# Performance work log

Hardware: AMD Instinct MI355X
Metric: run time of the kernel (lower is better)

The kernel has to match this reference:

```python
import jax, jax.numpy as jnp
import numpy as np

D_MODEL = 512
NHEAD = 8
DK = D_MODEL // NHEAD
DIM_FF = 2048
LN_EPS = 1e-5


def setup_inputs() -> dict:
    key = jax.random.key(0)
    ks = jax.random.split(key, 12)
    B, L = 8, 1024
    s = 1.0 / np.sqrt(D_MODEL)
    sf = 1.0 / np.sqrt(DIM_FF)
    return {
        "x": jax.random.normal(ks[0], (B, L, D_MODEL), jnp.float32),
        "key_padding_mask": jnp.zeros((B, L), dtype=bool),
        "bias": jax.random.normal(ks[1], (B, L, L), jnp.float32),
        # projection weights stored [in, out] so y = x @ W + b (matches torch Linear math)
        "Wq": jax.random.normal(ks[2], (D_MODEL, D_MODEL), jnp.float32) * s,
        "bq": jnp.zeros((D_MODEL,), jnp.float32),
        "Wk": jax.random.normal(ks[3], (D_MODEL, D_MODEL), jnp.float32) * s,
        "bk": jnp.zeros((D_MODEL,), jnp.float32),
        "Wv": jax.random.normal(ks[4], (D_MODEL, D_MODEL), jnp.float32) * s,
        "bv": jnp.zeros((D_MODEL,), jnp.float32),
        "Wo": jax.random.normal(ks[5], (D_MODEL, D_MODEL), jnp.float32) * s,
        "bo": jnp.zeros((D_MODEL,), jnp.float32),
        "ln1_g": jnp.ones((D_MODEL,), jnp.float32),
        "ln1_b": jnp.zeros((D_MODEL,), jnp.float32),
        "W1": jax.random.normal(ks[6], (D_MODEL, DIM_FF), jnp.float32) * s,
        "b1": jnp.zeros((DIM_FF,), jnp.float32),
        "W2": jax.random.normal(ks[7], (DIM_FF, D_MODEL), jnp.float32) * sf,
        "b2": jnp.zeros((D_MODEL,), jnp.float32),
        "ln2_g": jnp.ones((D_MODEL,), jnp.float32),
        "ln2_b": jnp.zeros((D_MODEL,), jnp.float32),
    }


def _layernorm(x, g, b):
    mu = jnp.mean(x, axis=-1, keepdims=True)
    var = jnp.mean(jnp.square(x - mu), axis=-1, keepdims=True)
    return (x - mu) * jax.lax.rsqrt(var + LN_EPS) * g + b


def reference(x, key_padding_mask, bias, Wq, bq, Wk, bk, Wv, bv, Wo, bo,
              ln1_g, ln1_b, W1, b1, W2, b2, ln2_g, ln2_b):
    B, L, H = x.shape
    residual = x
    # [B, L, D] -> [B, nhead, L, dk]
    q = (x @ Wq + bq).reshape(B, L, NHEAD, DK).transpose(0, 2, 1, 3)
    k = (x @ Wk + bk).reshape(B, L, NHEAD, DK).transpose(0, 2, 1, 3)
    v = (x @ Wv + bv).reshape(B, L, NHEAD, DK).transpose(0, 2, 1, 3)
    scores = jnp.einsum("bhqd,bhkd->bhqk", q, k) / np.sqrt(DK)
    scores = scores + bias[:, None, :, :]
    scores = jnp.where(key_padding_mask[:, None, None, :], -jnp.inf, scores)
    attn = jax.nn.softmax(scores, axis=-1)  # dropout p=0 (eval)
    out = jnp.einsum("bhqk,bhkd->bhqd", attn, v)
    out = out.transpose(0, 2, 1, 3).reshape(B, L, H)
    out = out @ Wo + bo
    x = _layernorm(residual + out, ln1_g, ln1_b)
    residual = x
    h = jax.nn.relu(x @ W1 + b1)
    x = h @ W2 + b2
    return _layernorm(residual + x, ln2_g, ln2_b)
```

## Files before the change

kernel.cpp:

```cpp
#include <hip/hip_runtime.h>
#include <math.h>

#define NHEAD 8
#define DKD 64
#define DMODEL 512
#define LSEQ 1024
#define NBL 8192

typedef __attribute__((ext_vector_type(8))) short bf8;
typedef __attribute__((ext_vector_type(4))) float f4;

__device__ inline unsigned short f2bf(float f) {
    union { float f; unsigned u; } v; v.f = f;
    unsigned r = v.u + 0x7FFFu + ((v.u >> 16) & 1u);
    return (unsigned short)(r >> 16);
}

__device__ __forceinline__ unsigned cvtpk(float lo, float hi) {
    unsigned r;
    asm("v_cvt_pk_bf16_f32 %0, %1, %2" : "=v"(r) : "v"(lo), "v"(hi));
    return r;
}

__device__ __forceinline__ void gload16(const void* g, void* l) {
    __builtin_amdgcn_global_load_lds(
        (const __attribute__((address_space(1))) unsigned int*)g,
        (__attribute__((address_space(3))) unsigned int*)l, 16, 0, 0);
}

__global__ __launch_bounds__(256) void conv_bf16(
    const float* __restrict__ in, unsigned short* __restrict__ out, int n)
{
    int i = (blockIdx.x * 256 + threadIdx.x) * 4;
    if (i >= n) return;
    float4 v = *(const float4*)(in + i);
    ushort4 o;
    o.x = f2bf(v.x); o.y = f2bf(v.y); o.z = f2bf(v.z); o.w = f2bf(v.w);
    *(ushort4*)(out + i) = o;
}

__global__ __launch_bounds__(256) void biasmb_kernel(
    const float* __restrict__ bias, const unsigned char* __restrict__ mask,
    unsigned short* __restrict__ o)
{
    size_t flat = ((size_t)blockIdx.x * 256 + threadIdx.x) * 8;
    int b = (int)(flat >> 20);
    int k = (int)(flat & 1023);
    float4 v0 = *(const float4*)(bias + flat);
    float4 v1 = *(const float4*)(bias + flat + 4);
    uint2 mk = *(const uint2*)(mask + b * 1024 + k);
    float vs[8] = {v0.x, v0.y, v0.z, v0.w, v1.x, v1.y, v1.z, v1.w};
    unsigned mw[2] = {mk.x, mk.y};
    unsigned short os[8];
    #pragma unroll
    for (int j = 0; j < 8; ++j) {
        unsigned mb = (mw[j >> 2] >> ((j & 3) * 8)) & 0xffu;
        os[j] = f2bf(mb ? -1e30f : vs[j]);
    }
    uint4 pk;
    pk.x = (unsigned)os[0] | ((unsigned)os[1] << 16);
    pk.y = (unsigned)os[2] | ((unsigned)os[3] << 16);
    pk.z = (unsigned)os[4] | ((unsigned)os[5] << 16);
    pk.w = (unsigned)os[6] | ((unsigned)os[7] << 16);
    *(uint4*)(o + flat) = pk;
}

__device__ __forceinline__ void do_transpose(
    const float* __restrict__ W, unsigned short* __restrict__ Wt,
    int K, int N, int bx, int by)
{
    __shared__ float tile[64][65];
    const int k0 = by * 64, n0 = bx * 64;
    const int c = threadIdx.x & 63, r0 = (threadIdx.x >> 6) * 16;
    #pragma unroll
    for (int i = 0; i < 16; ++i)
        tile[r0 + i][c] = W[(size_t)(k0 + r0 + i) * N + n0 + c];
    __syncthreads();
    #pragma unroll
    for (int i = 0; i < 16; ++i)
        Wt[(size_t)(n0 + r0 + i) * K + k0 + c] = f2bf(tile[c][r0 + i]);
}

__global__ __launch_bounds__(256) void prep_weights(
    const float* __restrict__ Wq, const float* __restrict__ Wk,
    const float* __restrict__ Wv, const float* __restrict__ Wo,
    const float* __restrict__ W1, const float* __restrict__ W2,
    const float* __restrict__ bq, const float* __restrict__ bk,
    const float* __restrict__ bv,
    unsigned short* __restrict__ Wqkv, unsigned short* __restrict__ Wot,
    unsigned short* __restrict__ W1t, unsigned short* __restrict__ W2t,
    float* __restrict__ bqkv)
{
    int j = blockIdx.x;
    if (j < 256) {
        int which = j >> 6, tt = j & 63;
        const float* src = which == 0 ? Wq : which == 1 ? Wk : which == 2 ? Wv : Wo;
        unsigned short* dst = which == 0 ? Wqkv : which == 1 ? (Wqkv + 262144)
                            : which == 2 ? (Wqkv + 524288) : Wot;
        do_transpose(src, dst, 512, 512, tt & 7, tt >> 3);
    } else if (j < 512) {
        int tt = j - 256;
        do_transpose(W1, W1t, 512, 2048, tt & 31, tt >> 5);
    } else if (j < 768) {
        int tt = j - 512;
        do_transpose(W2, W2t, 2048, 512, tt & 7, tt >> 3);
    } else {
        for (int c = threadIdx.x; c < 1536; c += 256)
            bqkv[c] = c < 512 ? bq[c] : c < 1024 ? bk[c - 512] : bv[c - 1024];
    }
}

template<int BN>
__global__ __launch_bounds__(256) void mfma_gemm(
    const unsigned short* __restrict__ A, const unsigned short* __restrict__ Bt,
    const float* __restrict__ bias, const float* __restrict__ resid,
    void* __restrict__ outp, int M, int N, int K, int relu, int outmode,
    unsigned short* __restrict__ qs, unsigned short* __restrict__ ks,
    unsigned short* __restrict__ vts)
{
    __shared__ uint4 As[2][1024];
    __shared__ uint4 Bs[2][BN * 8];
    constexpr int NB = BN / 32;

    const int t = threadIdx.x;
    const int lane = t & 63, w = t >> 6;
    const int g = lane >> 4, r15 = lane & 15;
    const int wr = w >> 1, wc = w & 1;

    const int nwg  = gridDim.x * gridDim.y;
    const int flat = blockIdx.y * gridDim.x + blockIdx.x;
    const int swz  = (flat & 7) * (nwg >> 3) + (flat >> 3);
    const int bx   = swz % gridDim.x, by = swz / gridDim.x;
    const int rowBase = by * 128, colBase = bx * BN;

    f4 acc[4][NB] = {};

    const int r   = t >> 3;
    const int chs = (t & 7) ^ (r & 7);
    const unsigned short* Ag0 = A  + (size_t)(rowBase + r) * K + chs * 8;
    const unsigned short* Bg0 = Bt + (size_t)(colBase + r) * K + chs * 8;

    auto stage = [&](int buf, int k0) {
        unsigned short* Al = (unsigned short*)As[buf] + (w * 8) * 64;
        unsigned short* Bl = (unsigned short*)Bs[buf] + (w * 8) * 64;
        const unsigned short* Ag = Ag0 + k0;
        const unsigned short* Bg = Bg0 + k0;
        #pragma unroll
        for (int p = 0; p < 4; ++p)
            gload16(Ag + (size_t)(p * 32) * K, Al + p * 32 * 64);
        #pragma unroll
        for (int p = 0; p < NB; ++p)
            gload16(Bg + (size_t)(p * 32) * K, Bl + p * 32 * 64);
    };

    const int nst = K >> 6;
    stage(0, 0);
    __syncthreads();

    for (int it = 0; it < nst; ++it) {
        const int cur = it & 1;
        if (it + 1 < nst) stage(cur ^ 1, (it + 1) << 6);
        #pragma unroll
        for (int kk = 0; kk < 2; ++kk) {
            bf8 af[4], bfr[NB];
            #pragma unroll
            for (int m = 0; m < 4; ++m) {
                int ra = wr * 64 + m * 16 + r15;
                af[m] = *(const bf8*)&As[cur][ra * 8 + ((kk * 4 + g) ^ (ra & 7))];
            }
            #pragma unroll
            for (int n = 0; n < NB; ++n) {
                int rb = wc * (BN / 2) + n * 16 + r15;
                bfr[n] = *(const bf8*)&Bs[cur][rb * 8 + ((kk * 4 + g) ^ (rb & 7))];
            }
            #pragma unroll
            for (int m = 0; m < 4; ++m)
                #pragma unroll
                for (int n = 0; n < NB; ++n)
                    acc[m][n] = __builtin_amdgcn_mfma_f32_16x16x32_bf16(
                        af[m], bfr[n], acc[m][n], 0, 0, 0);
        }
        __syncthreads();
    }

    #pragma unroll
    for (int m = 0; m < 4; ++m) {
        #pragma unroll
        for (int n = 0; n < NB; ++n) {
            int col = colBase + wc * (BN / 2) + n * 16 + r15;
            float bv = bias[col];
            #pragma unroll
            for (int rr = 0; rr < 4; ++rr) {
                int row = rowBase + wr * 64 + m * 16 + g * 4 + rr;
                float v = acc[m][n][rr] + bv;
                if (relu) v = fmaxf(v, 0.f);
                if (outmode == 0) {
                    size_t idx = (size_t)row * N + col;
                    if (resid) v += resid[idx];
                    ((float*)outp)[idx] = v;
                } else if (outmode == 1) {
                    ((unsigned short*)outp)[(size_t)row * N + col] = f2bf(v);
                } else {
                    int sel = col >> 9, hd = col & 511;
                    int h = hd >> 6, dk = hd & 63;
                    int b = row >> 10, l = row & 1023;
                    unsigned short bw = f2bf(v);
                    size_t bh = (size_t)(b * NHEAD + h);
                    if (sel == 0)      qs[(bh * LSEQ + l) * DKD + dk] = bw;
                    else if (sel == 1) ks[(bh * LSEQ + l) * DKD + dk] = bw;
                    else               vts[(bh * DKD + dk) * LSEQ + l] = bw;
                }
            }
        }
    }
}

__global__ __launch_bounds__(256) void attn_mfma(
    const unsigned short* __restrict__ Qg, const unsigned short* __restrict__ Kg,
    const unsigned short* __restrict__ Vtg, const unsigned short* __restrict__ biasMb,
    unsigned short* __restrict__ Ob)
{
    __shared__ uint4 Ks[2][512];
    __shared__ uint4 Vs[2][512];
    __shared__ uint4 Bls[2][1024];
    __shared__ unsigned int Pb[4096];

    const int t = threadIdx.x;
    const int lane = t & 63, w = t >> 6;
    const int g = lane >> 4, r15 = lane & 15;

    const int p = blockIdx.x;
    const int logical = (p & 7) * 64 + (p >> 3);
    const int bh = logical >> 3, qt = logical & 7;
    const int b = bh >> 3, h = bh & 7;
    const int qbase = qt * 128 + w * 32;

    bf8 qf[2][2];
    #pragma unroll
    for (int u = 0; u < 2; ++u) {
        const unsigned short* qp = Qg + ((size_t)bh * LSEQ + qbase + u * 16 + r15) * DKD + g * 8;
        qf[u][0] = *(const bf8*)qp;
        qf[u][1] = *(const bf8*)(qp + 32);
    }

    float mrun[2] = {-1e30f, -1e30f}, lsum[2] = {0.f, 0.f};
    f4 oacc[2][4] = {};

    const int sr   = t >> 3;
    const int chs  = (t & 7) ^ (sr & 7);
    const int brow = lane >> 3;
    const int bch  = (lane & 7) ^ brow;
    unsigned short* Pw = (unsigned short*)(Pb + w * 1024);

    const size_t kBase = (size_t)bh * LSEQ * DKD;
    const size_t vBase = (size_t)bh * DKD * LSEQ;
    const unsigned short* bB = biasMb + ((size_t)b << 20);

    auto stage = [&](int buf, int key0) {
        const unsigned short* Kgp = Kg  + kBase + (size_t)(key0 + sr) * DKD + chs * 8;
        const unsigned short* Vgp = Vtg + vBase + (size_t)sr * LSEQ + key0 + chs * 8;
        unsigned short* Kl = (unsigned short*)Ks[buf] + (w * 8) * 64;
        unsigned short* Vl = (unsigned short*)Vs[buf] + (w * 8) * 64;
        gload16(Kgp, Kl);
        gload16(Kgp + (size_t)32 * DKD, Kl + 32 * 64);
        gload16(Vgp, Vl);
        gload16(Vgp + (size_t)32 * LSEQ, Vl + 32 * 64);
        unsigned short* Bl = (unsigned short*)Bls[buf] + w * 2048;
        #pragma unroll
        for (int pp = 0; pp < 4; ++pp) {
            const unsigned short* Bgp = bB + (size_t)(qbase + pp * 8 + brow) * 1024
                                      + key0 + bch * 8;
            gload16(Bgp, Bl + pp * 512);
        }
    };

    stage(0, 0);
    __syncthreads();

    for (int kt = 0; kt < 16; ++kt) {
        const int cur = kt & 1;
        if (kt < 15) stage(cur ^ 1, (kt + 1) * 64);

        const char* Bw = (const char*)Bls[cur] + w * 4096;

        f4 sacc[2][4] = {};
        __builtin_amdgcn_s_setprio(1);
        #pragma unroll
        for (int kk = 0; kk < 2; ++kk)
            #pragma unroll
            for (int m = 0; m < 4; ++m) {
                int row = m * 16 + r15;
                bf8 kf = *(const bf8*)&Ks[cur][row * 8 + ((kk * 4 + g) ^ (row & 7))];
                sacc[0][m] = __builtin_amdgcn_mfma_f32_16x16x32_bf16(kf, qf[0][kk], sacc[0][m], 0, 0, 0);
                sacc[1][m] = __builtin_amdgcn_mfma_f32_16x16x32_bf16(kf, qf[1][kk], sacc[1][m], 0, 0, 0);
            }
        __builtin_amdgcn_s_setprio(0);

        #pragma unroll
        for (int u = 0; u < 2; ++u) {
            float s[16];
            float pmax = -1e30f;
            #pragma unroll
            for (int m = 0; m < 4; ++m) {
                int off = (u * 16 + r15) * 128 + ((m * 32 + g * 8) ^ ((r15 & 7) << 4));
                uint2 bv = *(const uint2*)(Bw + off);
                float b0 = __uint_as_float(bv.x << 16);
                float b1 = __uint_as_float(bv.x & 0xffff0000u);
                float b2 = __uint_as_float(bv.y << 16);
                float b3 = __uint_as_float(bv.y & 0xffff0000u);
                s[m * 4 + 0] = fmaf(sacc[u][m][0], 0.125f, b0);
                s[m * 4 + 1] = fmaf(sacc[u][m][1], 0.125f, b1);
                s[m * 4 + 2] = fmaf(sacc[u][m][2], 0.125f, b2);
                s[m * 4 + 3] = fmaf(sacc[u][m][3], 0.125f, b3);
                #pragma unroll
                for (int j = 0; j < 4; ++j) pmax = fmaxf(pmax, s[m * 4 + j]);
            }
            pmax = fmaxf(pmax, __shfl_xor(pmax, 16));
            pmax = fmaxf(pmax, __shfl_xor(pmax, 32));

            if (!__all(pmax <= mrun[u] + 8.f)) {
                float mnew = fmaxf(mrun[u], pmax);
                float scale = __expf(mrun[u] - mnew);
                lsum[u] *= scale;
                #pragma unroll
                for (int m = 0; m < 4; ++m)
                    #pragma unroll
                    for (int j = 0; j < 4; ++j) oacc[u][m][j] *= scale;
                mrun[u] = mnew;
            }

            float psum = 0.f;
            #pragma unroll
            for (int i = 0; i < 16; ++i) { s[i] = __expf(s[i] - mrun[u]); psum += s[i]; }
            psum += __shfl_xor(psum, 16);
            psum += __shfl_xor(psum, 32);
            lsum[u] += psum;

            #pragma unroll
            for (int m = 0; m < 4; ++m) {
                uint2 pk;
                pk.x = cvtpk(s[m * 4 + 0], s[m * 4 + 1]);
                pk.y = cvtpk(s[m * 4 + 2], s[m * 4 + 3]);
                int off = ((u * 16 + r15) * 128 + m * 32 + g * 8) ^ ((r15 & 7) << 4);
                *(uint2*)((char*)Pw + off) = pk;
            }
        }

        #pragma unroll
        for (int kk = 0; kk < 2; ++kk) {
            bf8 pf[2];
            #pragma unroll
            for (int u = 0; u < 2; ++u) {
                int off = ((u * 16 + r15) * 128 + kk * 64 + g * 16) ^ ((r15 & 7) << 4);
                pf[u] = *(const bf8*)((char*)Pw + off);
            }
            __builtin_amdgcn_s_setprio(1);
            #pragma unroll
            for (int m = 0; m < 4; ++m) {
                int row = m * 16 + r15;
                bf8 vf = *(const bf8*)&Vs[cur][row * 8 + ((kk * 4 + g) ^ (row & 7))];
                oacc[0][m] = __builtin_amdgcn_mfma_f32_16x16x32_bf16(vf, pf[0], oacc[0][m], 0, 0, 0);
                oacc[1][m] = __builtin_amdgcn_mfma_f32_16x16x32_bf16(vf, pf[1], oacc[1][m], 0, 0, 0);
            }
            __builtin_amdgcn_s_setprio(0);
        }
        __syncthreads();
    }

    #pragma unroll
    for (int u = 0; u < 2; ++u) {
        float inv = 1.f / lsum[u];
        unsigned short* op = Ob + ((size_t)b * LSEQ + qbase + u * 16 + r15) * DMODEL + h * DKD;
        #pragma unroll
        for (int m = 0; m < 4; ++m) {
            ushort4 o4;
            o4.x = f2bf(oacc[u][m][0] * inv);
            o4.y = f2bf(oacc[u][m][1] * inv);
            o4.z = f2bf(oacc[u][m][2] * inv);
            o4.w = f2bf(oacc[u][m][3] * inv);
            *(ushort4*)(op + m * 16 + g * 4) = o4;
        }
    }
}

__global__ __launch_bounds__(256) void ln_kernel(
    const float* __restrict__ in, const float* __restrict__ g,
    const float* __restrict__ bt, float* __restrict__ out,
    unsigned short* __restrict__ outb)
{
    const int row  = blockIdx.x * 4 + (threadIdx.x >> 6);
    const int lane = threadIdx.x & 63;
    const float* rp = in + (size_t)row * DMODEL + lane * 8;
    float4 x0 = *(const float4*)rp;
    float4 x1 = *(const float4*)(rp + 4);
    float xs[8] = {x0.x, x0.y, x0.z, x0.w, x1.x, x1.y, x1.z, x1.w};

    float sum = 0.f;
    #pragma unroll
    for (int i = 0; i < 8; ++i) sum += xs[i];
    #pragma unroll
    for (int off = 32; off; off >>= 1) sum += __shfl_xor(sum, off);
    float mu = sum * (1.f / 512.f);

    float vs = 0.f;
    #pragma unroll
    for (int i = 0; i < 8; ++i) { float d = xs[i] - mu; vs += d * d; }
    #pragma unroll
    for (int off = 32; off; off >>= 1) vs += __shfl_xor(vs, off);
    float rs = rsqrtf(vs * (1.f / 512.f) + 1e-5f);

    const float* gp = g  + lane * 8;
    const float* bp = bt + lane * 8;
    float4 g0 = *(const float4*)gp, g1 = *(const float4*)(gp + 4);
    float4 b0 = *(const float4*)bp, b1 = *(const float4*)(bp + 4);
    float gs[8] = {g0.x, g0.y, g0.z, g0.w, g1.x, g1.y, g1.z, g1.w};
    float bs[8] = {b0.x, b0.y, b0.z, b0.w, b1.x, b1.y, b1.z, b1.w};

    float res[8];
    #pragma unroll
    for (int i = 0; i < 8; ++i) res[i] = (xs[i] - mu) * rs * gs[i] + bs[i];

    float* op = out + (size_t)row * DMODEL + lane * 8;
    float4 r0 = {res[0], res[1], res[2], res[3]};
    float4 r1 = {res[4], res[5], res[6], res[7]};
    *(float4*)op       = r0;
    *(float4*)(op + 4) = r1;

    if (outb) {
        unsigned short* ob = outb + (size_t)row * DMODEL + lane * 8;
        ushort4 u0, u1;
        u0.x = f2bf(res[0]); u0.y = f2bf(res[1]); u0.z = f2bf(res[2]); u0.w = f2bf(res[3]);
        u1.x = f2bf(res[4]); u1.y = f2bf(res[5]); u1.z = f2bf(res[6]); u1.w = f2bf(res[7]);
        *(ushort4*)ob       = u0;
        *(ushort4*)(ob + 4) = u1;
    }
}

extern "C" void kernel_launch(void* const* d_in, const int* in_sizes, int n_in,
                              void* d_out, int out_size, void* d_ws, size_t ws_size,
                              hipStream_t stream)
{
    const float*         x    = (const float*)d_in[0];
    const unsigned char* mask = (const unsigned char*)d_in[1];
    const float*         bias = (const float*)d_in[2];
    const float* Wq = (const float*)d_in[3];
    const float* bq = (const float*)d_in[4];
    const float* Wk = (const float*)d_in[5];
    const float* bk = (const float*)d_in[6];
    const float* Wv = (const float*)d_in[7];
    const float* bv = (const float*)d_in[8];
    const float* Wo = (const float*)d_in[9];
    const float* bo = (const float*)d_in[10];
    const float* ln1g = (const float*)d_in[11];
    const float* ln1b = (const float*)d_in[12];
    const float* W1 = (const float*)d_in[13];
    const float* b1 = (const float*)d_in[14];
    const float* W2 = (const float*)d_in[15];
    const float* b2 = (const float*)d_in[16];
    const float* ln2g = (const float*)d_in[17];
    const float* ln2b = (const float*)d_in[18];

    char* W = (char*)d_ws;
    unsigned short* Qb   = (unsigned short*)(W);
    unsigned short* Kb   = (unsigned short*)(W + (8u << 20));
    unsigned short* Vtb  = (unsigned short*)(W + (16u << 20));
    unsigned short* Oball= (unsigned short*)(W + (24u << 20));
    unsigned short* hb   = (unsigned short*)(W);
    unsigned short* biasMb=(unsigned short*)(W + (32u << 20));
    float*          y12  = (float*)(W + (32u << 20));
    float*          x1   = (float*)(W + (49u << 20));
    unsigned short* xb   = (unsigned short*)(W + (66u << 20));
    unsigned short* x1b  = xb;
    unsigned short* Wqkv = (unsigned short*)(W + (74u << 20));
    unsigned short* Wot  = (unsigned short*)(W + (76u << 20));
    unsigned short* W1t  = (unsigned short*)(W + (77u << 20));
    unsigned short* W2t  = (unsigned short*)(W + (79u << 20));
    float*          bqkv = (float*)(W + (81u << 20));
    float*          outp = (float*)d_out;

    conv_bf16<<<dim3(4096), dim3(256), 0, stream>>>(x, xb, NBL * DMODEL);
    prep_weights<<<dim3(769), dim3(256), 0, stream>>>(
        Wq, Wk, Wv, Wo, W1, W2, bq, bk, bv, Wqkv, Wot, W1t, W2t, bqkv);
    biasmb_kernel<<<dim3(4096), dim3(256), 0, stream>>>(bias, mask, biasMb);

    mfma_gemm<128><<<dim3(12, 64), dim3(256), 0, stream>>>(
        xb, Wqkv, bqkv, nullptr, nullptr, NBL, 1536, 512, 0, 2, Qb, Kb, Vtb);

    attn_mfma<<<dim3(512), dim3(256), 0, stream>>>(Qb, Kb, Vtb, biasMb, Oball);

    mfma_gemm<64><<<dim3(8, 64), dim3(256), 0, stream>>>(
        Oball, Wot, bo, x, y12, NBL, 512, 512, 0, 0, nullptr, nullptr, nullptr);

    ln_kernel<<<dim3(NBL / 4), dim3(256), 0, stream>>>(y12, ln1g, ln1b, x1, x1b);

    mfma_gemm<128><<<dim3(16, 64), dim3(256), 0, stream>>>(
        x1b, W1t, b1, nullptr, hb, NBL, 2048, 512, 1, 1, nullptr, nullptr, nullptr);

    mfma_gemm<64><<<dim3(8, 64), dim3(256), 0, stream>>>(
        hb, W2t, b2, x1, y12, NBL, 512, 2048, 0, 0, nullptr, nullptr, nullptr);

    ln_kernel<<<dim3(NBL / 4), dim3(256), 0, stream>>>(y12, ln2g, ln2b, outp, nullptr);
}
```

Before: 327.9 us.

## Merge prep kernels, triple-buffer GEMM loads, and narrow GEMM tiles to BN=64

Folds the x conversion, bias/mask conversion and weight transposes into one launch, removing two kernel launches. The GEMM moves from double to triple buffering, using explicit vmcnt waits with raw s_barrier and raising wave priority around the MFMA block so loads stay further ahead of compute. The QKV and FFN1 GEMMs switch from 128-wide to 64-wide column tiles with twice as many blocks. Risks include more LDS per block, which may cut occupancy, and less reuse per narrower tile.

```diff
diff --git a/kernel.cpp b/kernel.cpp
--- a/kernel.cpp
+++ b/kernel.cpp
@@ -26,43 +26,6 @@
     __builtin_amdgcn_global_load_lds(
         (const __attribute__((address_space(1))) unsigned int*)g,
         (__attribute__((address_space(3))) unsigned int*)l, 16, 0, 0);
-}
-
-__global__ __launch_bounds__(256) void conv_bf16(
-    const float* __restrict__ in, unsigned short* __restrict__ out, int n)
-{
-    int i = (blockIdx.x * 256 + threadIdx.x) * 4;
-    if (i >= n) return;
-    float4 v = *(const float4*)(in + i);
-    ushort4 o;
-    o.x = f2bf(v.x); o.y = f2bf(v.y); o.z = f2bf(v.z); o.w = f2bf(v.w);
-    *(ushort4*)(out + i) = o;
-}
-
-__global__ __launch_bounds__(256) void biasmb_kernel(
-    const float* __restrict__ bias, const unsigned char* __restrict__ mask,
-    unsigned short* __restrict__ o)
-{
-    size_t flat = ((size_t)blockIdx.x * 256 + threadIdx.x) * 8;
-    int b = (int)(flat >> 20);
-    int k = (int)(flat & 1023);
-    float4 v0 = *(const float4*)(bias + flat);
-    float4 v1 = *(const float4*)(bias + flat + 4);
-    uint2 mk = *(const uint2*)(mask + b * 1024 + k);
-    float vs[8] = {v0.x, v0.y, v0.z, v0.w, v1.x, v1.y, v1.z, v1.w};
-    unsigned mw[2] = {mk.x, mk.y};
-    unsigned short os[8];
-    #pragma unroll
-    for (int j = 0; j < 8; ++j) {
-        unsigned mb = (mw[j >> 2] >> ((j & 3) * 8)) & 0xffu;
-        os[j] = f2bf(mb ? -1e30f : vs[j]);
-    }
-    uint4 pk;
-    pk.x = (unsigned)os[0] | ((unsigned)os[1] << 16);
-    pk.y = (unsigned)os[2] | ((unsigned)os[3] << 16);
-    pk.z = (unsigned)os[4] | ((unsigned)os[5] << 16);
-    pk.w = (unsigned)os[6] | ((unsigned)os[7] << 16);
-    *(uint4*)(o + flat) = pk;
 }
 
 __device__ __forceinline__ void do_transpose(
@@ -81,7 +44,10 @@
         Wt[(size_t)(n0 + r0 + i) * K + k0 + c] = f2bf(tile[c][r0 + i]);
 }
 
-__global__ __launch_bounds__(256) void prep_weights(
+__global__ __launch_bounds__(256) void prep_all(
+    const float* __restrict__ x, unsigned short* __restrict__ xb,
+    const float* __restrict__ bias, const unsigned char* __restrict__ mask,
+    unsigned short* __restrict__ biasMb,
     const float* __restrict__ Wq, const float* __restrict__ Wk,
     const float* __restrict__ Wv, const float* __restrict__ Wo,
     const float* __restrict__ W1, const float* __restrict__ W2,
@@ -91,22 +57,52 @@
     unsigned short* __restrict__ W1t, unsigned short* __restrict__ W2t,
     float* __restrict__ bqkv)
 {
-    int j = blockIdx.x;
-    if (j < 256) {
-        int which = j >> 6, tt = j & 63;
-        const float* src = which == 0 ? Wq : which == 1 ? Wk : which == 2 ? Wv : Wo;
-        unsigned short* dst = which == 0 ? Wqkv : which == 1 ? (Wqkv + 262144)
-                            : which == 2 ? (Wqkv + 524288) : Wot;
-        do_transpose(src, dst, 512, 512, tt & 7, tt >> 3);
-    } else if (j < 512) {
-        int tt = j - 256;
-        do_transpose(W1, W1t, 512, 2048, tt & 31, tt >> 5);
-    } else if (j < 768) {
-        int tt = j - 512;
-        do_transpose(W2, W2t, 2048, 512, tt & 7, tt >> 3);
+    const int j = blockIdx.x;
+    if (j < 4096) {
+        int i = (j * 256 + threadIdx.x) * 4;
+        float4 v = *(const float4*)(x + i);
+        ushort4 o;
+        o.x = f2bf(v.x); o.y = f2bf(v.y); o.z = f2bf(v.z); o.w = f2bf(v.w);
+        *(ushort4*)(xb + i) = o;
+    } else if (j < 8192) {
+        size_t flat = ((size_t)(j - 4096) * 256 + threadIdx.x) * 8;
+        int b = (int)(flat >> 20);
+        int k = (int)(flat & 1023);
+        float4 v0 = *(const float4*)(bias + flat);
+        float4 v1 = *(const float4*)(bias + flat + 4);
+        uint2 mk = *(const uint2*)(mask + b * 1024 + k);
+        float vs[8] = {v0.x, v0.y, v0.z, v0.w, v1.x, v1.y, v1.z, v1.w};
+        unsigned mw[2] = {mk.x, mk.y};
+        unsigned short os[8];
+        #pragma unroll
+        for (int q = 0; q < 8; ++q) {
+            unsigned mb = (mw[q >> 2] >> ((q & 3) * 8)) & 0xffu;
+            os[q] = f2bf(mb ? -1e30f : vs[q]);
+        }
+        uint4 pk;
+        pk.x = (unsigned)os[0] | ((unsigned)os[1] << 16);
+        pk.y = (unsigned)os[2] | ((unsigned)os[3] << 16);
+        pk.z = (unsigned)os[4] | ((unsigned)os[5] << 16);
+        pk.w = (unsigned)os[6] | ((unsigned)os[7] << 16);
+        *(uint4*)(biasMb + flat) = pk;
     } else {
-        for (int c = threadIdx.x; c < 1536; c += 256)
-            bqkv[c] = c < 512 ? bq[c] : c < 1024 ? bk[c - 512] : bv[c - 1024];
+        int jj = j - 8192;
+        if (jj < 256) {
+            int which = jj >> 6, tt = jj & 63;
+            const float* src = which == 0 ? Wq : which == 1 ? Wk : which == 2 ? Wv : Wo;
+            unsigned short* dst = which == 0 ? Wqkv : which == 1 ? (Wqkv + 262144)
+                                : which == 2 ? (Wqkv + 524288) : Wot;
+            do_transpose(src, dst, 512, 512, tt & 7, tt >> 3);
+        } else if (jj < 512) {
+            int tt = jj - 256;
+            do_transpose(W1, W1t, 512, 2048, tt & 31, tt >> 5);
+        } else if (jj < 768) {
+            int tt = jj - 512;
+            do_transpose(W2, W2t, 2048, 512, tt & 7, tt >> 3);
+        } else {
+            for (int c = threadIdx.x; c < 1536; c += 256)
+                bqkv[c] = c < 512 ? bq[c] : c < 1024 ? bk[c - 512] : bv[c - 1024];
+        }
     }
 }
 
@@ -118,8 +114,8 @@
     unsigned short* __restrict__ qs, unsigned short* __restrict__ ks,
     unsigned short* __restrict__ vts)
 {
-    __shared__ uint4 As[2][1024];
-    __shared__ uint4 Bs[2][BN * 8];
+    __shared__ uint4 As[3][1024];
+    __shared__ uint4 Bs[3][BN * 8];
     constexpr int NB = BN / 32;
 
     const int t = threadIdx.x;
@@ -155,11 +151,20 @@
 
     const int nst = K >> 6;
     stage(0, 0);
-    __syncthreads();
+    stage(1, 64);
 
     for (int it = 0; it < nst; ++it) {
-        const int cur = it & 1;
-        if (it + 1 < nst) stage(cur ^ 1, (it + 1) << 6);
+        const int cur = it % 3;
+        if (it + 1 < nst) {
+            if constexpr (BN == 128) asm volatile("s_waitcnt vmcnt(8)" ::: "memory");
+            else                     asm volatile("s_waitcnt vmcnt(6)" ::: "memory");
+        } else {
+            asm volatile("s_waitcnt vmcnt(0)" ::: "memory");
+        }
+        __builtin_amdgcn_sched_barrier(0);
+        __builtin_amdgcn_s_barrier();
+        if (it + 2 < nst) stage((it + 2) % 3, (it + 2) << 6);
+
         #pragma unroll
         for (int kk = 0; kk < 2; ++kk) {
             bf8 af[4], bfr[NB];
@@ -173,14 +178,16 @@
                 int rb = wc * (BN / 2) + n * 16 + r15;
                 bfr[n] = *(const bf8*)&Bs[cur][rb * 8 + ((kk * 4 + g) ^ (rb & 7))];
             }
+            __builtin_amdgcn_s_setprio(1);
             #pragma unroll
             for (int m = 0; m < 4; ++m)
                 #pragma unroll
                 for (int n = 0; n < NB; ++n)
                     acc[m][n] = __builtin_amdgcn_mfma_f32_16x16x32_bf16(
                         af[m], bfr[n], acc[m][n], 0, 0, 0);
-        }
-        __syncthreads();
+            __builtin_amdgcn_s_setprio(0);
+        }
+        __builtin_amdgcn_s_barrier();
     }
 
     #pragma unroll
@@ -478,12 +485,11 @@
     float*          bqkv = (float*)(W + (81u << 20));
     float*          outp = (float*)d_out;
 
-    conv_bf16<<<dim3(4096), dim3(256), 0, stream>>>(x, xb, NBL * DMODEL);
-    prep_weights<<<dim3(769), dim3(256), 0, stream>>>(
-        Wq, Wk, Wv, Wo, W1, W2, bq, bk, bv, Wqkv, Wot, W1t, W2t, bqkv);
-    biasmb_kernel<<<dim3(4096), dim3(256), 0, stream>>>(bias, mask, biasMb);
-
-    mfma_gemm<128><<<dim3(12, 64), dim3(256), 0, stream>>>(
+    prep_all<<<dim3(8961), dim3(256), 0, stream>>>(
+        x, xb, bias, mask, biasMb, Wq, Wk, Wv, Wo, W1, W2,
+        bq, bk, bv, Wqkv, Wot, W1t, W2t, bqkv);
+
+    mfma_gemm<64><<<dim3(24, 64), dim3(256), 0, stream>>>(
         xb, Wqkv, bqkv, nullptr, nullptr, NBL, 1536, 512, 0, 2, Qb, Kb, Vtb);
 
     attn_mfma<<<dim3(512), dim3(256), 0, stream>>>(Qb, Kb, Vtb, biasMb, Oball);
@@ -493,7 +499,7 @@
 
     ln_kernel<<<dim3(NBL / 4), dim3(256), 0, stream>>>(y12, ln1g, ln1b, x1, x1b);
 
-    mfma_gemm<128><<<dim3(16, 64), dim3(256), 0, stream>>>(
+    mfma_gemm<64><<<dim3(32, 64), dim3(256), 0, stream>>>(
         x1b, W1t, b1, nullptr, hb, NBL, 2048, 512, 1, 1, nullptr, nullptr, nullptr);
 
     mfma_gemm<64><<<dim3(8, 64), dim3(256), 0, stream>>>(
```

Result: no change. 327.8 us (-0.1%).
